# Kernel tuning notes

Hardware: AMD Instinct MI355X
Metric: run time of the kernel (lower is better)

## Reference

```python
import jax, jax.numpy as jnp
import numpy as np

N_NODES = 100000
N_EDGES = 3200000
D_IN = 256
D_OUT = 256


def setup_inputs() -> dict:
    key = jax.random.key(0)
    k1, k2, k3, k4, k5 = jax.random.split(key, 5)
    input_feature = jax.random.normal(k1, (N_NODES, D_IN), dtype=jnp.float32)
    edge_row = jax.random.randint(k2, (N_EDGES,), 0, N_NODES, dtype=jnp.int32)
    edge_col = jax.random.randint(k3, (N_EDGES,), 0, N_NODES, dtype=jnp.int32)
    edge_val = jax.random.uniform(k4, (N_EDGES,), dtype=jnp.float32)
    # xavier_uniform for weight [D_IN, D_OUT]
    limit = float(np.sqrt(6.0 / (D_IN + D_OUT)))
    weight = jax.random.uniform(k5, (D_IN, D_OUT), minval=-limit, maxval=limit, dtype=jnp.float32)
    bias = jnp.zeros((D_OUT,), dtype=jnp.float32)
    return {
        "input_feature": input_feature,
        "edge_row": edge_row,
        "edge_col": edge_col,
        "edge_val": edge_val,
        "weight": weight,
        "bias": bias,
    }


def reference(input_feature, edge_row, edge_col, edge_val, weight, bias):
    # support = X @ W   [N, D_OUT]
    support = input_feature @ weight
    # output[i] = sum_{(i,j) in E} A[i,j] * support[j]  (sparse adjacency SpMM)
    messages = edge_val[:, None] * support[edge_col]  # [E, D_OUT]
    output = jax.ops.segment_sum(messages, edge_row, num_segments=N_NODES)
    return output + bias
```

## Files before the change

kernel.cpp:

```cpp
#include <hip/hip_runtime.h>

#define N_NODES 100000
#define N_EDGES 3200000
#define DIM 256

#define BROWS 256
#define NBUCK 391

typedef short short8 __attribute__((ext_vector_type(8)));
typedef float f32x4 __attribute__((ext_vector_type(4)));

static __device__ __forceinline__ unsigned short f2bf(float f) {
    unsigned int u = __float_as_uint(f);
    u = (u + 0x7FFFu + ((u >> 16) & 1u)) >> 16;
    return (unsigned short)u;
}

__global__ void k_hist(const int* __restrict__ row, int* __restrict__ cnt) {
    int e = blockIdx.x * 256 + threadIdx.x;
    atomicAdd(&cnt[row[e]], 1);
}

__global__ void k_scan1(const int* __restrict__ cnt, int* __restrict__ rs,
                        int* __restrict__ bsum) {
    __shared__ int lds[1024];
    int t = threadIdx.x;
    int g = blockIdx.x * 1024 + t;
    int x = cnt[g];
    lds[t] = x;
    __syncthreads();
    for (int off = 1; off < 1024; off <<= 1) {
        int v = (t >= off) ? lds[t - off] : 0;
        __syncthreads();
        lds[t] += v;
        __syncthreads();
    }
    rs[g] = lds[t] - x;
    if (t == 1023) bsum[blockIdx.x] = lds[t];
}

__global__ void k_scan2(int* __restrict__ bsum) {
    __shared__ int lds[128];
    int t = threadIdx.x;
    int x = (t < 98) ? bsum[t] : 0;
    lds[t] = x;
    __syncthreads();
    for (int off = 1; off < 128; off <<= 1) {
        int v = (t >= off) ? lds[t - off] : 0;
        __syncthreads();
        lds[t] += v;
        __syncthreads();
    }
    if (t < 98) bsum[t] = lds[t] - x;
}

__global__ void k_scanadd(int* __restrict__ rs, const int* __restrict__ bsum) {
    int g = blockIdx.x * 1024 + threadIdx.x;
    rs[g] = rs[g] + bsum[blockIdx.x];
}

__global__ void k_binit(const int* __restrict__ rs, int* __restrict__ bcur) {
    int t = threadIdx.x;
    if (t < NBUCK) bcur[t] = rs[t * BROWS];
}

__global__ __launch_bounds__(512) void k_bucket(const int* __restrict__ row,
                                                const int* __restrict__ col,
                                                const float* __restrict__ val,
                                                int* __restrict__ bcur,
                                                int2* __restrict__ tmp) {
    __shared__ int hist[NBUCK];
    __shared__ int base[NBUCK];
    int t = threadIdx.x;
    const int per = (N_EDGES + gridDim.x - 1) / gridDim.x;
    int e0 = blockIdx.x * per;
    int e1 = min(e0 + per, N_EDGES);
    for (int i = t; i < NBUCK; i += 512) hist[i] = 0;
    __syncthreads();
    for (int e = e0 + t; e < e1; e += 512)
        atomicAdd(&hist[row[e] >> 8], 1);
    __syncthreads();
    for (int i = t; i < NBUCK; i += 512) {
        int c = hist[i];
        base[i] = c ? atomicAdd(&bcur[i], c) : 0;
        hist[i] = 0;
    }
    __syncthreads();
    for (int e = e0 + t; e < e1; e += 512) {
        int r = row[e];
        int b = r >> 8;
        int off = atomicAdd(&hist[b], 1);
        tmp[base[b] + off] = make_int2(((r & 255) << 17) | col[e],
                                       __float_as_int(val[e]));
    }
}

__global__ __launch_bounds__(256) void k_place(const int* __restrict__ rs,
                                               const int2* __restrict__ tmp,
                                               int2* __restrict__ csr) {
    __shared__ int lcur[BROWS];
    int t = threadIdx.x;
    int rowbase = blockIdx.x * BROWS;
    int rr = rowbase + t;
    lcur[t] = (rr < N_NODES) ? rs[rr] : 0;
    __syncthreads();
    int s = rs[rowbase];
    int e = rs[min(rowbase + BROWS, N_NODES)];
    for (int i = s + t; i < e; i += 256) {
        int2 x = tmp[i];
        int pos = atomicAdd(&lcur[x.x >> 17], 1);
        csr[pos] = make_int2(x.x & 0x1FFFF, x.y);
    }
}

__global__ void k_wpack(const float* __restrict__ W, unsigned short* __restrict__ wp) {
    int t = blockIdx.x * 256 + threadIdx.x;
    int lane = t & 63;
    int nt = (t >> 6) & 15;
    int kc = t >> 10;
    int n = nt * 16 + (lane & 15);
    int kbase = kc * 32 + ((lane >> 4) << 3);
    unsigned short* dst = wp + (size_t)t * 8;
#pragma unroll
    for (int j = 0; j < 8; j++) dst[j] = f2bf(W[(size_t)(kbase + j) * DIM + n]);
}

#define LDSTRIDE 528
__global__ __launch_bounds__(1024, 4) void k_gemm(const float* __restrict__ X,
                                                  const unsigned short* __restrict__ wp,
                                                  unsigned short* __restrict__ sup) {
    __shared__ char pool[16 * 16 * LDSTRIDE];
    unsigned short* wlds = (unsigned short*)pool;
    int t = threadIdx.x;
    int wave = t >> 6, lane = t & 63;
    int q = lane >> 4, nl = lane & 15;

    const int nstrips = (N_NODES + 255) / 256;
    for (int s = blockIdx.x; s < nstrips; s += gridDim.x) {
        for (int i = t; i < 8192; i += 1024)
            ((uint4*)wlds)[i] = ((const uint4*)wp)[i];
        __syncthreads();

        int rowbase = s * 256 + wave * 16;
        f32x4 acc[16];
#pragma unroll
        for (int mt = 0; mt < 16; mt++) acc[mt] = (f32x4){0.f, 0.f, 0.f, 0.f};

        for (int kc = 0; kc < 8; kc++) {
            int r = rowbase + nl;
            short8 b = (short8)0;
            if (r < N_NODES) {
                const float* bp = X + (size_t)r * DIM + kc * 32 + (q << 3);
                float4 b0 = *(const float4*)bp;
                float4 b1 = *(const float4*)(bp + 4);
                b[0] = (short)f2bf(b0.x); b[1] = (short)f2bf(b0.y);
                b[2] = (short)f2bf(b0.z); b[3] = (short)f2bf(b0.w);
                b[4] = (short)f2bf(b1.x); b[5] = (short)f2bf(b1.y);
                b[6] = (short)f2bf(b1.z); b[7] = (short)f2bf(b1.w);
            }
#pragma unroll
            for (int mt = 0; mt < 16; mt++) {
                short8 a = *(const short8*)&wlds[(size_t)(((kc * 16 + mt) * 64) + lane) * 8];
                acc[mt] = __builtin_amdgcn_mfma_f32_16x16x32_bf16(a, b, acc[mt], 0, 0, 0);
            }
        }
        __syncthreads();

        char* wbase = pool + wave * (16 * LDSTRIDE);
#pragma unroll
        for (int mt = 0; mt < 16; mt++) {
            uint2 p;
            p.x = ((unsigned int)f2bf(acc[mt][1]) << 16) | f2bf(acc[mt][0]);
            p.y = ((unsigned int)f2bf(acc[mt][3]) << 16) | f2bf(acc[mt][2]);
            *(uint2*)(wbase + nl * LDSTRIDE + mt * 32 + q * 8) = p;
        }
#pragma unroll
        for (int i = 0; i < 8; i++) {
            int row = 2 * i + (lane >> 5);
            uint4 v = *(const uint4*)(wbase + row * LDSTRIDE + (lane & 31) * 16);
            int node = rowbase + row;
            if (node < N_NODES)
                *(uint4*)((char*)sup + (size_t)node * 512 + (lane & 31) * 16) = v;
        }
        __syncthreads();
    }
}

__global__ __launch_bounds__(256) void k_agg(const int* __restrict__ rs,
                                             const int2* __restrict__ csr,
                                             const unsigned short* __restrict__ sup,
                                             const float* __restrict__ bias,
                                             float* __restrict__ out) {
    int wave = threadIdx.x >> 6, lane = threadIdx.x & 63;
    int r = blockIdx.x * 4 + wave;
    int s = rs[r], e = rs[r + 1];
    int g = lane >> 4;
    int L = lane & 15;

    float acc[16];
#pragma unroll
    for (int j = 0; j < 16; j++) acc[j] = 0.f;

    int i = s;
    for (; i + 4 <= e; i += 4) {
        int2 ce = csr[i + g];
        float v = __int_as_float(ce.y);
        const uint4* sp = (const uint4*)(sup + (size_t)ce.x * DIM + L * 16);
        uint4 u0 = sp[0];
        uint4 u1 = sp[1];
        unsigned int uu[8] = {u0.x, u0.y, u0.z, u0.w, u1.x, u1.y, u1.z, u1.w};
#pragma unroll
        for (int k = 0; k < 8; k++) {
            acc[2 * k]     += v * __uint_as_float(uu[k] << 16);
            acc[2 * k + 1] += v * __uint_as_float(uu[k] & 0xFFFF0000u);
        }
    }
    {
        int idx = i + g;
        if (idx < e) {
            int2 ce = csr[idx];
            float v = __int_as_float(ce.y);
            const uint4* sp = (const uint4*)(sup + (size_t)ce.x * DIM + L * 16);
            uint4 u0 = sp[0];
            uint4 u1 = sp[1];
            unsigned int uu[8] = {u0.x, u0.y, u0.z, u0.w, u1.x, u1.y, u1.z, u1.w};
#pragma unroll
            for (int k = 0; k < 8; k++) {
                acc[2 * k]     += v * __uint_as_float(uu[k] << 16);
                acc[2 * k + 1] += v * __uint_as_float(uu[k] & 0xFFFF0000u);
            }
        }
    }
#pragma unroll
    for (int j = 0; j < 16; j++) {
        float x = acc[j];
        x += __shfl_down(x, 32, 64);
        x += __shfl_down(x, 16, 64);
        acc[j] = x;
    }
    if (lane < 16) {
        float4* op = (float4*)(out + (size_t)r * DIM + L * 16);
        const float4* bp = (const float4*)(bias + L * 16);
#pragma unroll
        for (int qq = 0; qq < 4; qq++) {
            float4 b = bp[qq];
            float4 o;
            o.x = acc[4 * qq]     + b.x;
            o.y = acc[4 * qq + 1] + b.y;
            o.z = acc[4 * qq + 2] + b.z;
            o.w = acc[4 * qq + 3] + b.w;
            op[qq] = o;
        }
    }
}

extern "C" void kernel_launch(void* const* d_in, const int* in_sizes, int n_in,
                              void* d_out, int out_size, void* d_ws, size_t ws_size,
                              hipStream_t stream) {
    const float* X    = (const float*)d_in[0];
    const int*   erow = (const int*)d_in[1];
    const int*   ecol = (const int*)d_in[2];
    const float* eval = (const float*)d_in[3];
    const float* W    = (const float*)d_in[4];
    const float* bias = (const float*)d_in[5];
    float* out = (float*)d_out;

    char* ws = (char*)d_ws;
    int*            rsb  = (int*)ws;
    int*            cur  = (int*)(ws + 409600);
    int*            bsum = (int*)(ws + 819200);
    int*            bcur = (int*)(ws + 819200) + 128;
    unsigned short* wp   = (unsigned short*)(ws + 823296);
    int2*           csr  = (int2*)(ws + 954368);
    unsigned short* sup  = (unsigned short*)(ws + 26554368);
    int2*           tmp  = (int2*)(ws + 26554368);

    hipMemsetAsync(cur, 0, 409600, stream);
    k_hist<<<N_EDGES / 256, 256, 0, stream>>>(erow, cur);
    k_scan1<<<98, 1024, 0, stream>>>(cur, rsb, bsum);
    k_scan2<<<1, 128, 0, stream>>>(bsum);
    k_scanadd<<<98, 1024, 0, stream>>>(rsb, bsum);
    k_binit<<<1, 512, 0, stream>>>(rsb, bcur);
    k_bucket<<<256, 512, 0, stream>>>(erow, ecol, eval, bcur, tmp);
    k_place<<<NBUCK, 256, 0, stream>>>(rsb, tmp, csr);
    k_wpack<<<32, 256, 0, stream>>>(W, wp);
    k_gemm<<<256, 1024, 0, stream>>>(X, wp, sup);
    k_agg<<<N_NODES / 4, 256, 0, stream>>>(rsb, csr, sup, bias, out);
}
```

Measured before the change: 672.5 us.

## Replace per-row CSR with bucketed partitions and LDS-accumulated aggregation

Drops the full per-row histogram and scan and builds 128-row buckets instead. Inside each bucket, edges are sorted by (row mod 16, column bin) so each of 16 waves owns a disjoint set of rows and walks edges in column-local order. Aggregation accumulates into a 128x256 fp32 LDS tile, so the support gathers get more cache locality and the per-row CSR construction goes away. In exchange each block uses 128 KB of LDS, which limits occupancy to one block per CU, and edge work can be imbalanced across waves.

```diff
diff --git a/kernel.cpp b/kernel.cpp
--- a/kernel.cpp
+++ b/kernel.cpp
@@ -4,8 +4,11 @@
 #define N_EDGES 3200000
 #define DIM 256
 
-#define BROWS 256
-#define NBUCK 391
+#define BROWS 128
+#define NBUCK 782
+#define NCBIN 49
+#define NPART 16
+#define NKEY (NPART * NCBIN)
 
 typedef short short8 __attribute__((ext_vector_type(8)));
 typedef float f32x4 __attribute__((ext_vector_type(4)));
@@ -16,17 +19,27 @@
     return (unsigned short)u;
 }
 
-__global__ void k_hist(const int* __restrict__ row, int* __restrict__ cnt) {
-    int e = blockIdx.x * 256 + threadIdx.x;
-    atomicAdd(&cnt[row[e]], 1);
-}
-
-__global__ void k_scan1(const int* __restrict__ cnt, int* __restrict__ rs,
-                        int* __restrict__ bsum) {
+__global__ __launch_bounds__(512) void k_cnt(const int* __restrict__ row,
+                                             int* __restrict__ bcnt) {
+    __shared__ int h[NBUCK];
+    int t = threadIdx.x;
+    const int per = N_EDGES / 256;
+    int e0 = blockIdx.x * per, e1 = e0 + per;
+    for (int i = t; i < NBUCK; i += 512) h[i] = 0;
+    __syncthreads();
+    for (int e = e0 + t; e < e1; e += 512)
+        atomicAdd(&h[row[e] >> 7], 1);
+    __syncthreads();
+    for (int i = t; i < NBUCK; i += 512)
+        if (h[i]) atomicAdd(&bcnt[i], h[i]);
+}
+
+__global__ __launch_bounds__(1024) void k_scanb(const int* __restrict__ bcnt,
+                                                int* __restrict__ bbase,
+                                                int* __restrict__ bcur) {
     __shared__ int lds[1024];
     int t = threadIdx.x;
-    int g = blockIdx.x * 1024 + t;
-    int x = cnt[g];
+    int x = (t < NBUCK) ? bcnt[t] : 0;
     lds[t] = x;
     __syncthreads();
     for (int off = 1; off < 1024; off <<= 1) {
@@ -35,50 +48,24 @@
         lds[t] += v;
         __syncthreads();
     }
-    rs[g] = lds[t] - x;
-    if (t == 1023) bsum[blockIdx.x] = lds[t];
-}
-
-__global__ void k_scan2(int* __restrict__ bsum) {
-    __shared__ int lds[128];
-    int t = threadIdx.x;
-    int x = (t < 98) ? bsum[t] : 0;
-    lds[t] = x;
-    __syncthreads();
-    for (int off = 1; off < 128; off <<= 1) {
-        int v = (t >= off) ? lds[t - off] : 0;
-        __syncthreads();
-        lds[t] += v;
-        __syncthreads();
-    }
-    if (t < 98) bsum[t] = lds[t] - x;
-}
-
-__global__ void k_scanadd(int* __restrict__ rs, const int* __restrict__ bsum) {
-    int g = blockIdx.x * 1024 + threadIdx.x;
-    rs[g] = rs[g] + bsum[blockIdx.x];
-}
-
-__global__ void k_binit(const int* __restrict__ rs, int* __restrict__ bcur) {
-    int t = threadIdx.x;
-    if (t < NBUCK) bcur[t] = rs[t * BROWS];
-}
-
-__global__ __launch_bounds__(512) void k_bucket(const int* __restrict__ row,
-                                                const int* __restrict__ col,
-                                                const float* __restrict__ val,
-                                                int* __restrict__ bcur,
-                                                int2* __restrict__ tmp) {
+    if (t < NBUCK) { int ex = lds[t] - x; bbase[t] = ex; bcur[t] = ex; }
+    if (t == 1023) bbase[NBUCK] = lds[1023];
+}
+
+__global__ __launch_bounds__(512) void k_bucket2(const int* __restrict__ row,
+                                                 const int* __restrict__ col,
+                                                 const float* __restrict__ val,
+                                                 int* __restrict__ bcur,
+                                                 int2* __restrict__ tmp) {
     __shared__ int hist[NBUCK];
     __shared__ int base[NBUCK];
     int t = threadIdx.x;
-    const int per = (N_EDGES + gridDim.x - 1) / gridDim.x;
-    int e0 = blockIdx.x * per;
-    int e1 = min(e0 + per, N_EDGES);
+    const int per = N_EDGES / 256;
+    int e0 = blockIdx.x * per, e1 = e0 + per;
     for (int i = t; i < NBUCK; i += 512) hist[i] = 0;
     __syncthreads();
     for (int e = e0 + t; e < e1; e += 512)
-        atomicAdd(&hist[row[e] >> 8], 1);
+        atomicAdd(&hist[row[e] >> 7], 1);
     __syncthreads();
     for (int i = t; i < NBUCK; i += 512) {
         int c = hist[i];
@@ -88,28 +75,47 @@
     __syncthreads();
     for (int e = e0 + t; e < e1; e += 512) {
         int r = row[e];
-        int b = r >> 8;
+        int b = r >> 7;
         int off = atomicAdd(&hist[b], 1);
-        tmp[base[b] + off] = make_int2(((r & 255) << 17) | col[e],
+        tmp[base[b] + off] = make_int2(((r & 127) << 17) | col[e],
                                        __float_as_int(val[e]));
     }
 }
 
-__global__ __launch_bounds__(256) void k_place(const int* __restrict__ rs,
-                                               const int2* __restrict__ tmp,
-                                               int2* __restrict__ csr) {
-    __shared__ int lcur[BROWS];
-    int t = threadIdx.x;
-    int rowbase = blockIdx.x * BROWS;
-    int rr = rowbase + t;
-    lcur[t] = (rr < N_NODES) ? rs[rr] : 0;
-    __syncthreads();
-    int s = rs[rowbase];
-    int e = rs[min(rowbase + BROWS, N_NODES)];
-    for (int i = s + t; i < e; i += 256) {
-        int2 x = tmp[i];
-        int pos = atomicAdd(&lcur[x.x >> 17], 1);
-        csr[pos] = make_int2(x.x & 0x1FFFF, x.y);
+__global__ __launch_bounds__(1024) void k_place2(const int* __restrict__ bbase,
+                                                 const int2* __restrict__ tmp,
+                                                 int2* __restrict__ csr2,
+                                                 int* __restrict__ pstart) {
+    __shared__ int h[1024];
+    __shared__ int cur[NKEY];
+    int t = threadIdx.x;
+    int b = blockIdx.x;
+    int s = bbase[b], e = bbase[b + 1];
+    h[t] = 0;
+    __syncthreads();
+    for (int i = s + t; i < e; i += 1024) {
+        int rx = tmp[i].x;
+        int key = ((rx >> 17) & 15) * NCBIN + ((rx & 0x1FFFF) >> 11);
+        atomicAdd(&h[key], 1);
+    }
+    __syncthreads();
+    int x = h[t];
+    __syncthreads();
+    for (int off = 1; off < 1024; off <<= 1) {
+        int v = (t >= off) ? h[t - off] : 0;
+        __syncthreads();
+        h[t] += v;
+        __syncthreads();
+    }
+    if (t < NKEY) cur[t] = s + h[t] - x;
+    __syncthreads();
+    if (t < NPART) pstart[b * NPART + t] = cur[t * NCBIN];
+    __syncthreads();
+    for (int i = s + t; i < e; i += 1024) {
+        int2 rec = tmp[i];
+        int key = ((rec.x >> 17) & 15) * NCBIN + ((rec.x & 0x1FFFF) >> 11);
+        int p = atomicAdd(&cur[key], 1);
+        csr2[p] = rec;
     }
 }
 
@@ -186,70 +192,55 @@
     }
 }
 
-__global__ __launch_bounds__(256) void k_agg(const int* __restrict__ rs,
-                                             const int2* __restrict__ csr,
-                                             const unsigned short* __restrict__ sup,
-                                             const float* __restrict__ bias,
-                                             float* __restrict__ out) {
-    int wave = threadIdx.x >> 6, lane = threadIdx.x & 63;
-    int r = blockIdx.x * 4 + wave;
-    int s = rs[r], e = rs[r + 1];
-    int g = lane >> 4;
-    int L = lane & 15;
-
-    float acc[16];
-#pragma unroll
-    for (int j = 0; j < 16; j++) acc[j] = 0.f;
-
-    int i = s;
-    for (; i + 4 <= e; i += 4) {
-        int2 ce = csr[i + g];
-        float v = __int_as_float(ce.y);
-        const uint4* sp = (const uint4*)(sup + (size_t)ce.x * DIM + L * 16);
-        uint4 u0 = sp[0];
-        uint4 u1 = sp[1];
-        unsigned int uu[8] = {u0.x, u0.y, u0.z, u0.w, u1.x, u1.y, u1.z, u1.w};
-#pragma unroll
-        for (int k = 0; k < 8; k++) {
-            acc[2 * k]     += v * __uint_as_float(uu[k] << 16);
-            acc[2 * k + 1] += v * __uint_as_float(uu[k] & 0xFFFF0000u);
-        }
-    }
-    {
-        int idx = i + g;
-        if (idx < e) {
-            int2 ce = csr[idx];
-            float v = __int_as_float(ce.y);
-            const uint4* sp = (const uint4*)(sup + (size_t)ce.x * DIM + L * 16);
-            uint4 u0 = sp[0];
-            uint4 u1 = sp[1];
-            unsigned int uu[8] = {u0.x, u0.y, u0.z, u0.w, u1.x, u1.y, u1.z, u1.w};
-#pragma unroll
-            for (int k = 0; k < 8; k++) {
-                acc[2 * k]     += v * __uint_as_float(uu[k] << 16);
-                acc[2 * k + 1] += v * __uint_as_float(uu[k] & 0xFFFF0000u);
-            }
-        }
-    }
-#pragma unroll
-    for (int j = 0; j < 16; j++) {
-        float x = acc[j];
-        x += __shfl_down(x, 32, 64);
-        x += __shfl_down(x, 16, 64);
-        acc[j] = x;
-    }
-    if (lane < 16) {
-        float4* op = (float4*)(out + (size_t)r * DIM + L * 16);
-        const float4* bp = (const float4*)(bias + L * 16);
-#pragma unroll
-        for (int qq = 0; qq < 4; qq++) {
-            float4 b = bp[qq];
+__global__ __launch_bounds__(1024) void k_agg2(const int* __restrict__ bbase,
+                                               const int* __restrict__ pstart,
+                                               const int2* __restrict__ csr2,
+                                               const unsigned short* __restrict__ sup,
+                                               const float* __restrict__ bias,
+                                               float* __restrict__ out) {
+    __shared__ float acc[BROWS * DIM];
+    int t = threadIdx.x;
+    int b = blockIdx.x;
+
+    float4* a4 = (float4*)acc;
+    for (int i = t; i < BROWS * (DIM / 4); i += 1024)
+        a4[i] = make_float4(0.f, 0.f, 0.f, 0.f);
+    __syncthreads();
+
+    int w = t >> 6, lane = t & 63;
+    int lo = bbase[b], hi = bbase[b + 1];
+    int s = pstart[b * NPART + w];
+    int e = (w < NPART - 1) ? pstart[b * NPART + w + 1] : hi;
+    s = max(s, lo); e = min(e, hi);
+
+#pragma unroll 2
+    for (int i = s; i < e; ++i) {
+        int2 rec = csr2[i];
+        int row = (rec.x >> 17) & 127;
+        float v = __int_as_float(rec.y);
+        const uint2* sp = (const uint2*)(sup + (size_t)(rec.x & 0x1FFFF) * DIM + lane * 4);
+        uint2 u = *sp;
+        float* ap = acc + row * DIM + lane * 4;
+        f32x4 a = *(f32x4*)ap;
+        a[0] += v * __uint_as_float(u.x << 16);
+        a[1] += v * __uint_as_float(u.x & 0xFFFF0000u);
+        a[2] += v * __uint_as_float(u.y << 16);
+        a[3] += v * __uint_as_float(u.y & 0xFFFF0000u);
+        *(f32x4*)ap = a;
+    }
+    __syncthreads();
+
+    int gr0 = b * BROWS;
+    for (int i = t; i < BROWS * (DIM / 4); i += 1024) {
+        int lr = i >> 6, c4 = i & 63;
+        int gr = gr0 + lr;
+        if (gr < N_NODES) {
+            float4 bv = ((const float4*)bias)[c4];
+            float4 av = a4[i];
             float4 o;
-            o.x = acc[4 * qq]     + b.x;
-            o.y = acc[4 * qq + 1] + b.y;
-            o.z = acc[4 * qq + 2] + b.z;
-            o.w = acc[4 * qq + 3] + b.w;
-            op[qq] = o;
+            o.x = av.x + bv.x; o.y = av.y + bv.y;
+            o.z = av.z + bv.z; o.w = av.w + bv.w;
+            ((float4*)out)[(size_t)gr * 64 + c4] = o;
         }
     }
 }
@@ -266,24 +257,21 @@
     float* out = (float*)d_out;
 
     char* ws = (char*)d_ws;
-    int*            rsb  = (int*)ws;
-    int*            cur  = (int*)(ws + 409600);
-    int*            bsum = (int*)(ws + 819200);
-    int*            bcur = (int*)(ws + 819200) + 128;
-    unsigned short* wp   = (unsigned short*)(ws + 823296);
-    int2*           csr  = (int2*)(ws + 954368);
-    unsigned short* sup  = (unsigned short*)(ws + 26554368);
-    int2*           tmp  = (int2*)(ws + 26554368);
-
-    hipMemsetAsync(cur, 0, 409600, stream);
-    k_hist<<<N_EDGES / 256, 256, 0, stream>>>(erow, cur);
-    k_scan1<<<98, 1024, 0, stream>>>(cur, rsb, bsum);
-    k_scan2<<<1, 128, 0, stream>>>(bsum);
-    k_scanadd<<<98, 1024, 0, stream>>>(rsb, bsum);
-    k_binit<<<1, 512, 0, stream>>>(rsb, bcur);
-    k_bucket<<<256, 512, 0, stream>>>(erow, ecol, eval, bcur, tmp);
-    k_place<<<NBUCK, 256, 0, stream>>>(rsb, tmp, csr);
+    int*            bcnt   = (int*)ws;
+    int*            bbase  = (int*)(ws + 4096);
+    int*            bcur   = (int*)(ws + 8192);
+    int*            pstart = (int*)(ws + 16384);
+    unsigned short* wp     = (unsigned short*)(ws + 823296);
+    int2*           csr2   = (int2*)(ws + 954368);
+    unsigned short* sup    = (unsigned short*)(ws + 26554368);
+    int2*           tmp    = (int2*)(ws + 26554368);
+
+    hipMemsetAsync(bcnt, 0, 4096, stream);
+    k_cnt<<<256, 512, 0, stream>>>(erow, bcnt);
+    k_scanb<<<1, 1024, 0, stream>>>(bcnt, bbase, bcur);
+    k_bucket2<<<256, 512, 0, stream>>>(erow, ecol, eval, bcur, tmp);
+    k_place2<<<NBUCK, 1024, 0, stream>>>(bbase, tmp, csr2, pstart);
     k_wpack<<<32, 256, 0, stream>>>(W, wp);
     k_gemm<<<256, 1024, 0, stream>>>(X, wp, sup);
-    k_agg<<<N_NODES / 4, 256, 0, stream>>>(rsb, csr, sup, bias, out);
-}
+    k_agg2<<<NBUCK, 1024, 0, stream>>>(bbase, pstart, csr2, sup, bias, out);
+}
```

After: 744.3 us. +10.7%, slower.

## Replace per-node global histogram and scan with bucket-level counts and local row scans

Applied to the files above, without the earlier changes.

Edges are now counted per 128-row bucket in shared memory rather than with a global per-node atomic histogram. A single small scan produces the bucket bases, and the placement kernel builds per-row offsets with a local histogram and scan inside each bucket. This removes the 3.2M global atomics, the multi-kernel scan, and several launches. In exchange, the placement kernel reads tmp twice and uses smaller buckets with 1024-thread blocks.

```diff
diff --git a/kernel.cpp b/kernel.cpp
--- a/kernel.cpp
+++ b/kernel.cpp
@@ -4,8 +4,8 @@
 #define N_EDGES 3200000
 #define DIM 256
 
-#define BROWS 256
-#define NBUCK 391
+#define BROWS 128
+#define NBUCK 782
 
 typedef short short8 __attribute__((ext_vector_type(8)));
 typedef float f32x4 __attribute__((ext_vector_type(4)));
@@ -16,17 +16,28 @@
     return (unsigned short)u;
 }
 
-__global__ void k_hist(const int* __restrict__ row, int* __restrict__ cnt) {
-    int e = blockIdx.x * 256 + threadIdx.x;
-    atomicAdd(&cnt[row[e]], 1);
-}
-
-__global__ void k_scan1(const int* __restrict__ cnt, int* __restrict__ rs,
-                        int* __restrict__ bsum) {
+__global__ __launch_bounds__(512) void k_cnt(const int* __restrict__ row,
+                                             int* __restrict__ bcnt) {
+    __shared__ int h[NBUCK];
+    int t = threadIdx.x;
+    const int per = N_EDGES / 256;
+    int e0 = blockIdx.x * per, e1 = e0 + per;
+    for (int i = t; i < NBUCK; i += 512) h[i] = 0;
+    __syncthreads();
+    for (int e = e0 + t; e < e1; e += 512)
+        atomicAdd(&h[row[e] >> 7], 1);
+    __syncthreads();
+    for (int i = t; i < NBUCK; i += 512)
+        if (h[i]) atomicAdd(&bcnt[i], h[i]);
+}
+
+__global__ __launch_bounds__(1024) void k_scanb(const int* __restrict__ bcnt,
+                                                int* __restrict__ bbase,
+                                                int* __restrict__ bcur,
+                                                int* __restrict__ rs) {
     __shared__ int lds[1024];
     int t = threadIdx.x;
-    int g = blockIdx.x * 1024 + t;
-    int x = cnt[g];
+    int x = (t < NBUCK) ? bcnt[t] : 0;
     lds[t] = x;
     __syncthreads();
     for (int off = 1; off < 1024; off <<= 1) {
@@ -35,50 +46,24 @@
         lds[t] += v;
         __syncthreads();
     }
-    rs[g] = lds[t] - x;
-    if (t == 1023) bsum[blockIdx.x] = lds[t];
-}
-
-__global__ void k_scan2(int* __restrict__ bsum) {
-    __shared__ int lds[128];
-    int t = threadIdx.x;
-    int x = (t < 98) ? bsum[t] : 0;
-    lds[t] = x;
-    __syncthreads();
-    for (int off = 1; off < 128; off <<= 1) {
-        int v = (t >= off) ? lds[t - off] : 0;
-        __syncthreads();
-        lds[t] += v;
-        __syncthreads();
-    }
-    if (t < 98) bsum[t] = lds[t] - x;
-}
-
-__global__ void k_scanadd(int* __restrict__ rs, const int* __restrict__ bsum) {
-    int g = blockIdx.x * 1024 + threadIdx.x;
-    rs[g] = rs[g] + bsum[blockIdx.x];
-}
-
-__global__ void k_binit(const int* __restrict__ rs, int* __restrict__ bcur) {
-    int t = threadIdx.x;
-    if (t < NBUCK) bcur[t] = rs[t * BROWS];
-}
-
-__global__ __launch_bounds__(512) void k_bucket(const int* __restrict__ row,
-                                                const int* __restrict__ col,
-                                                const float* __restrict__ val,
-                                                int* __restrict__ bcur,
-                                                int2* __restrict__ tmp) {
+    if (t < NBUCK) { int ex = lds[t] - x; bbase[t] = ex; bcur[t] = ex; }
+    if (t == 1023) { bbase[NBUCK] = lds[1023]; rs[N_NODES] = N_EDGES; }
+}
+
+__global__ __launch_bounds__(512) void k_bucket2(const int* __restrict__ row,
+                                                 const int* __restrict__ col,
+                                                 const float* __restrict__ val,
+                                                 int* __restrict__ bcur,
+                                                 int2* __restrict__ tmp) {
     __shared__ int hist[NBUCK];
     __shared__ int base[NBUCK];
     int t = threadIdx.x;
-    const int per = (N_EDGES + gridDim.x - 1) / gridDim.x;
-    int e0 = blockIdx.x * per;
-    int e1 = min(e0 + per, N_EDGES);
+    const int per = N_EDGES / 256;
+    int e0 = blockIdx.x * per, e1 = e0 + per;
     for (int i = t; i < NBUCK; i += 512) hist[i] = 0;
     __syncthreads();
     for (int e = e0 + t; e < e1; e += 512)
-        atomicAdd(&hist[row[e] >> 8], 1);
+        atomicAdd(&hist[row[e] >> 7], 1);
     __syncthreads();
     for (int i = t; i < NBUCK; i += 512) {
         int c = hist[i];
@@ -88,28 +73,46 @@
     __syncthreads();
     for (int e = e0 + t; e < e1; e += 512) {
         int r = row[e];
-        int b = r >> 8;
+        int b = r >> 7;
         int off = atomicAdd(&hist[b], 1);
-        tmp[base[b] + off] = make_int2(((r & 255) << 17) | col[e],
+        tmp[base[b] + off] = make_int2(((r & 127) << 17) | col[e],
                                        __float_as_int(val[e]));
     }
 }
 
-__global__ __launch_bounds__(256) void k_place(const int* __restrict__ rs,
-                                               const int2* __restrict__ tmp,
-                                               int2* __restrict__ csr) {
-    __shared__ int lcur[BROWS];
-    int t = threadIdx.x;
-    int rowbase = blockIdx.x * BROWS;
-    int rr = rowbase + t;
-    lcur[t] = (rr < N_NODES) ? rs[rr] : 0;
-    __syncthreads();
-    int s = rs[rowbase];
-    int e = rs[min(rowbase + BROWS, N_NODES)];
-    for (int i = s + t; i < e; i += 256) {
-        int2 x = tmp[i];
-        int pos = atomicAdd(&lcur[x.x >> 17], 1);
-        csr[pos] = make_int2(x.x & 0x1FFFF, x.y);
+__global__ __launch_bounds__(1024) void k_place3(const int* __restrict__ bbase,
+                                                 const int2* __restrict__ tmp,
+                                                 int2* __restrict__ csr,
+                                                 int* __restrict__ rs) {
+    __shared__ int h[BROWS];
+    __shared__ int cur[BROWS];
+    int t = threadIdx.x;
+    int b = blockIdx.x;
+    int s = bbase[b], e = bbase[b + 1];
+    if (t < BROWS) h[t] = 0;
+    __syncthreads();
+    for (int i = s + t; i < e; i += 1024)
+        atomicAdd(&h[(tmp[i].x >> 17) & 127], 1);
+    __syncthreads();
+    int x = (t < BROWS) ? h[t] : 0;
+    __syncthreads();
+    for (int off = 1; off < BROWS; off <<= 1) {
+        int v = (t >= off && t < BROWS) ? h[t - off] : 0;
+        __syncthreads();
+        if (t < BROWS) h[t] += v;
+        __syncthreads();
+    }
+    if (t < BROWS) {
+        int ex = s + h[t] - x;
+        cur[t] = ex;
+        int rr = b * BROWS + t;
+        if (rr < N_NODES) rs[rr] = ex;
+    }
+    __syncthreads();
+    for (int i = s + t; i < e; i += 1024) {
+        int2 rec = tmp[i];
+        int p = atomicAdd(&cur[(rec.x >> 17) & 127], 1);
+        csr[p] = make_int2(rec.x & 0x1FFFF, rec.y);
     }
 }
 
@@ -266,24 +269,21 @@
     float* out = (float*)d_out;
 
     char* ws = (char*)d_ws;
-    int*            rsb  = (int*)ws;
-    int*            cur  = (int*)(ws + 409600);
-    int*            bsum = (int*)(ws + 819200);
-    int*            bcur = (int*)(ws + 819200) + 128;
-    unsigned short* wp   = (unsigned short*)(ws + 823296);
-    int2*           csr  = (int2*)(ws + 954368);
-    unsigned short* sup  = (unsigned short*)(ws + 26554368);
-    int2*           tmp  = (int2*)(ws + 26554368);
-
-    hipMemsetAsync(cur, 0, 409600, stream);
-    k_hist<<<N_EDGES / 256, 256, 0, stream>>>(erow, cur);
-    k_scan1<<<98, 1024, 0, stream>>>(cur, rsb, bsum);
-    k_scan2<<<1, 128, 0, stream>>>(bsum);
-    k_scanadd<<<98, 1024, 0, stream>>>(rsb, bsum);
-    k_binit<<<1, 512, 0, stream>>>(rsb, bcur);
-    k_bucket<<<256, 512, 0, stream>>>(erow, ecol, eval, bcur, tmp);
-    k_place<<<NBUCK, 256, 0, stream>>>(rsb, tmp, csr);
+    int*            rs    = (int*)ws;
+    int*            bcnt  = (int*)(ws + 409600);
+    int*            bbase = (int*)(ws + 413696);
+    int*            bcur  = (int*)(ws + 417792);
+    unsigned short* wp    = (unsigned short*)(ws + 823296);
+    int2*           csr   = (int2*)(ws + 954368);
+    unsigned short* sup   = (unsigned short*)(ws + 26554368);
+    int2*           tmp   = (int2*)(ws + 26554368);
+
+    hipMemsetAsync(bcnt, 0, 4096, stream);
+    k_cnt<<<256, 512, 0, stream>>>(erow, bcnt);
+    k_scanb<<<1, 1024, 0, stream>>>(bcnt, bbase, bcur, rs);
+    k_bucket2<<<256, 512, 0, stream>>>(erow, ecol, eval, bcur, tmp);
+    k_place3<<<NBUCK, 1024, 0, stream>>>(bbase, tmp, csr, rs);
     k_wpack<<<32, 256, 0, stream>>>(W, wp);
     k_gemm<<<256, 1024, 0, stream>>>(X, wp, sup);
-    k_agg<<<N_NODES / 4, 256, 0, stream>>>(rsb, csr, sup, bias, out);
-}
+    k_agg<<<N_NODES / 4, 256, 0, stream>>>(rs, csr, sup, bias, out);
+}
```

New measurement: 558.2 us. 1.2x faster.
